# Optimization experiments

Measured on AMD Instinct MI355X. Metric: run time of the kernel, lower is better.

## Reference

```python
import jax, jax.numpy as jnp
import numpy as np

N = 8192
F_IN, F_HID, F_OUT = 256, 256, 64


def setup_inputs() -> dict:
    key = jax.random.key(0)
    k1, k2, k3, k4 = jax.random.split(key, 4)
    adj = jax.random.uniform(k1, (N, N), dtype=jnp.float32)
    x = jax.random.normal(k2, (N, F_IN), dtype=jnp.float32)
    W1 = jax.random.uniform(k3, (F_IN, F_HID), dtype=jnp.float32)
    W2 = jax.random.uniform(k4, (F_HID, F_OUT), dtype=jnp.float32)
    return {"adj": adj, "x": x, "W1": W1, "W2": W2}


def reference(adj, x, W1, W2):
    # Layer 1: left_to_right -> (adj @ x) @ W1, then ReLU (dropout is identity in eval)
    h = jnp.matmul(jnp.matmul(adj, x), W1)
    h = jax.nn.relu(h)
    # Layer 2 (last): no activation
    h = jnp.matmul(jnp.matmul(adj, h), W2)
    # Final log_softmax over class dim
    return jax.nn.log_softmax(h, axis=1)
```

## Files before the change

kernel.cpp:

```cpp
#include <hip/hip_runtime.h>

typedef short bf16x8 __attribute__((ext_vector_type(8)));
typedef float f32x4 __attribute__((ext_vector_type(4)));
typedef unsigned short us8 __attribute__((ext_vector_type(8)));

__device__ __forceinline__ unsigned short f2bf(float f) {
    unsigned int u = __float_as_uint(f);
    u += 0x7fffu + ((u >> 16) & 1u);
    return (unsigned short)(u >> 16);
}

__global__ __launch_bounds__(256) void transpose_cast_kernel(
    const float* __restrict__ in, unsigned short* __restrict__ out, int R, int Cc) {
    __shared__ alignas(16) unsigned short sT[64][65];
    const int r0 = blockIdx.x * 64, c0 = blockIdx.y * 64;
    const int t = threadIdx.x;
#pragma unroll
    for (int p = 0; p < 16; ++p) {
        int flat = p * 256 + t;
        int r = flat >> 6, c = flat & 63;
        sT[c][r] = f2bf(in[(size_t)(r0 + r) * Cc + (c0 + c)]);
    }
    __syncthreads();
#pragma unroll
    for (int p = 0; p < 16; ++p) {
        int flat = p * 256 + t;
        int c = flat >> 6, r = flat & 63;
        out[(size_t)(c0 + c) * R + (r0 + r)] = sT[c][r];
    }
}

template<int BN, int WM, int WN, int AMODE, bool TOUT, typename OutT>
__global__ __launch_bounds__(256) void gemm_kernel(
    const void* __restrict__ Aptr, const unsigned short* __restrict__ BT,
    OutT* __restrict__ C, int M, int N, int K, long aslab) {
    constexpr int BM = 64, BK = 64, LDW = 72;
    constexpr int MF = BM / WM / 16;
    constexpr int NF = BN / WN / 16;
    __shared__ alignas(16) unsigned short sA[BM * LDW];
    __shared__ alignas(16) unsigned short sB[BN * LDW];
    const int t = threadIdx.x;
    const int w = t >> 6, l = t & 63;
    const int wr = w / WN, wc = w % WN;
    const int m0 = blockIdx.x * BM;
    const int klen = K / gridDim.z;
    const int kbeg = blockIdx.z * klen;
    OutT* Cp = C + (size_t)blockIdx.z * M * N;

    f32x4 acc[MF][NF] = {};

    for (int k0 = kbeg; k0 < kbeg + klen; k0 += BK) {
        const float* A32 = (const float*)Aptr;
#pragma unroll
        for (int p = 0; p < 4; ++p) {
            int flat = p * 256 + t;
            int row = flat >> 4, c4 = flat & 15;
            size_t base = (size_t)(m0 + row) * K + k0 + c4 * 4;
            float4 v = *(const float4*)&A32[base];
            if constexpr (AMODE == 2) {
                float4 b = *(const float4*)&A32[aslab + base];
                float4 c = *(const float4*)&A32[2 * aslab + base];
                float4 d = *(const float4*)&A32[3 * aslab + base];
                v.x = fmaxf(v.x + b.x + c.x + d.x, 0.f);
                v.y = fmaxf(v.y + b.y + c.y + d.y, 0.f);
                v.z = fmaxf(v.z + b.z + c.z + d.z, 0.f);
                v.w = fmaxf(v.w + b.w + c.w + d.w, 0.f);
            }
            ushort4 o = make_ushort4(f2bf(v.x), f2bf(v.y), f2bf(v.z), f2bf(v.w));
            *(ushort4*)&sA[row * LDW + c4 * 4] = o;
        }
#pragma unroll
        for (int p = 0; p < BN * 8 / 256; ++p) {
            int flat = p * 256 + t;
            int row = flat >> 3, c8 = flat & 7;
            us8 v = *(const us8*)&BT[(size_t)row * K + k0 + c8 * 8];
            *(us8*)&sB[row * LDW + c8 * 8] = v;
        }
        __syncthreads();
#pragma unroll
        for (int kk = 0; kk < BK; kk += 32) {
            bf16x8 av[MF], bv[NF];
#pragma unroll
            for (int m = 0; m < MF; ++m)
                av[m] = *(const bf16x8*)&sA[(wr * (BM / WM) + m * 16 + (l & 15)) * LDW + kk + (l >> 4) * 8];
#pragma unroll
            for (int n = 0; n < NF; ++n)
                bv[n] = *(const bf16x8*)&sB[(wc * (BN / WN) + n * 16 + (l & 15)) * LDW + kk + (l >> 4) * 8];
#pragma unroll
            for (int m = 0; m < MF; ++m)
#pragma unroll
                for (int n = 0; n < NF; ++n)
                    acc[m][n] = __builtin_amdgcn_mfma_f32_16x16x32_bf16(av[m], bv[n], acc[m][n], 0, 0, 0);
        }
        __syncthreads();
    }

#pragma unroll
    for (int m = 0; m < MF; ++m) {
#pragma unroll
        for (int n = 0; n < NF; ++n) {
            const int col = wc * (BN / WN) + n * 16 + (l & 15);
            const int rb = m0 + wr * (BM / WM) + m * 16 + ((l >> 4) << 2);
            float v0 = acc[m][n][0], v1 = acc[m][n][1], v2 = acc[m][n][2], v3 = acc[m][n][3];
            if constexpr (TOUT) {
                ushort4 o = make_ushort4(f2bf(v0), f2bf(v1), f2bf(v2), f2bf(v3));
                *(ushort4*)((unsigned short*)Cp + (size_t)col * M + rb) = o;
            } else {
                Cp[(size_t)(rb + 0) * N + col] = (OutT)v0;
                Cp[(size_t)(rb + 1) * N + col] = (OutT)v1;
                Cp[(size_t)(rb + 2) * N + col] = (OutT)v2;
                Cp[(size_t)(rb + 3) * N + col] = (OutT)v3;
            }
        }
    }
}

template<int BN, int THREADS, int WM, int WN>
__global__ __launch_bounds__(THREADS, 4) void big_gemm_kernel(
    const float* __restrict__ A, const unsigned short* __restrict__ BT,
    float* __restrict__ C, int M, int N, int K) {
    constexpr int BM = 128, BK = 64, LDW = 72;
    constexpr int MF = BM / WM / 16, NF = BN / WN / 16;
    constexpr int ACH = (BM * BK / 4) / THREADS;
    constexpr int BCH = (BN * BK / 8) / THREADS;
    __shared__ alignas(16) unsigned short sA[2][BM * LDW];
    __shared__ alignas(16) unsigned short sB[2][BN * LDW];
    const int t = threadIdx.x, w = t >> 6, l = t & 63;
    const int wr = w / WN, wc = w % WN;
    const int m0 = blockIdx.x * BM;
    const int klen = K / gridDim.z, kbeg = blockIdx.z * klen;
    const int NT = klen / BK;
    float* Cp = C + (size_t)blockIdx.z * M * N;

    float4 ar[ACH];
    us8 br[BCH];

    auto LOAD = [&](int kc) {
#pragma unroll
        for (int p = 0; p < ACH; ++p) {
            int flat = p * THREADS + t, row = flat >> 4, c4 = flat & 15;
            ar[p] = *(const float4*)&A[(size_t)(m0 + row) * K + kc + c4 * 4];
        }
#pragma unroll
        for (int p = 0; p < BCH; ++p) {
            int flat = p * THREADS + t, row = flat >> 3, c8 = flat & 7;
            br[p] = *(const us8*)&BT[(size_t)row * K + kc + c8 * 8];
        }
    };
    auto WRITE = [&](int buf) {
#pragma unroll
        for (int p = 0; p < ACH; ++p) {
            int flat = p * THREADS + t, row = flat >> 4, c4 = flat & 15;
            float4 v = ar[p];
            *(ushort4*)&sA[buf][row * LDW + c4 * 4] =
                make_ushort4(f2bf(v.x), f2bf(v.y), f2bf(v.z), f2bf(v.w));
        }
#pragma unroll
        for (int p = 0; p < BCH; ++p) {
            int flat = p * THREADS + t, row = flat >> 3, c8 = flat & 7;
            *(us8*)&sB[buf][row * LDW + c8 * 8] = br[p];
        }
    };

    f32x4 acc[MF][NF] = {};
    LOAD(kbeg);
    WRITE(0);
    __syncthreads();
    int cur = 0;
    for (int tt = 0; tt < NT; ++tt) {
        if (tt + 1 < NT) LOAD(kbeg + (tt + 1) * BK);
#pragma unroll
        for (int kk = 0; kk < BK; kk += 32) {
            bf16x8 av[MF], bv[NF];
#pragma unroll
            for (int m = 0; m < MF; ++m)
                av[m] = *(const bf16x8*)&sA[cur][(wr * (BM / WM) + m * 16 + (l & 15)) * LDW + kk + (l >> 4) * 8];
#pragma unroll
            for (int n = 0; n < NF; ++n)
                bv[n] = *(const bf16x8*)&sB[cur][(wc * (BN / WN) + n * 16 + (l & 15)) * LDW + kk + (l >> 4) * 8];
#pragma unroll
            for (int m = 0; m < MF; ++m)
#pragma unroll
                for (int n = 0; n < NF; ++n)
                    acc[m][n] = __builtin_amdgcn_mfma_f32_16x16x32_bf16(av[m], bv[n], acc[m][n], 0, 0, 0);
        }
        if (tt + 1 < NT) {
            WRITE(cur ^ 1);
            __syncthreads();
            cur ^= 1;
        }
    }
#pragma unroll
    for (int m = 0; m < MF; ++m)
#pragma unroll
        for (int n = 0; n < NF; ++n) {
            const int col = wc * (BN / WN) + n * 16 + (l & 15);
            const int rb = m0 + wr * (BM / WM) + m * 16 + ((l >> 4) << 2);
#pragma unroll
            for (int j = 0; j < 4; ++j)
                Cp[(size_t)(rb + j) * N + col] = acc[m][n][j];
        }
}

__global__ __launch_bounds__(256) void head2_kernel(
    const float* __restrict__ p, float* __restrict__ out, int M) {
    const int t = threadIdx.x, w = t >> 6, l = t & 63;
    const size_t stride = (size_t)M * 64;
#pragma unroll
    for (int rr = 0; rr < 4; ++rr) {
        int i = blockIdx.x * 16 + w * 4 + rr;
        size_t off = (size_t)i * 64 + l;
        float v = 0.f;
#pragma unroll
        for (int s = 0; s < 8; ++s) v += p[s * stride + off];
        float mx = v;
#pragma unroll
        for (int o = 32; o; o >>= 1) mx = fmaxf(mx, __shfl_xor(mx, o));
        float d0 = v - mx;
        float e = __expf(d0);
#pragma unroll
        for (int o = 32; o; o >>= 1) e += __shfl_xor(e, o);
        out[off] = d0 - __logf(e);
    }
}

extern "C" void kernel_launch(void* const* d_in, const int* in_sizes, int n_in,
                              void* d_out, int out_size, void* d_ws, size_t ws_size,
                              hipStream_t stream) {
    const float* adj = (const float*)d_in[0];
    const float* x   = (const float*)d_in[1];
    const float* W1  = (const float*)d_in[2];
    const float* W2  = (const float*)d_in[3];
    float* out = (float*)d_out;

    const int M = 8192, K = 8192;
    char* ws = (char*)d_ws;
    float*          pbuf1 = (float*)ws;
    float*          pbuf2 = (float*)(ws + 33554432);
    unsigned short* zT    = (unsigned short*)(ws + 50331648);
    unsigned short* hwT   = (unsigned short*)(ws + 54525952);
    unsigned short* W1T   = (unsigned short*)(ws + 55574528);
    unsigned short* W2T   = (unsigned short*)(ws + 55705600);

    transpose_cast_kernel<<<dim3(4, 4), 256, 0, stream>>>(W1, W1T, 256, 256);
    transpose_cast_kernel<<<dim3(4, 1), 256, 0, stream>>>(W2, W2T, 256, 64);
    gemm_kernel<256, 1, 4, 1, true, unsigned short>
        <<<dim3(M / 64, 1, 1), 256, 0, stream>>>(x, W1T, zT, M, 256, 256, 0);
    big_gemm_kernel<256, 1024, 4, 4>
        <<<dim3(M / 128, 1, 4), 1024, 0, stream>>>(adj, zT, pbuf1, M, 256, K);
    gemm_kernel<64, 2, 2, 2, true, unsigned short>
        <<<dim3(M / 64, 1, 1), 256, 0, stream>>>(pbuf1, W2T, hwT, M, 64, 256, (long)M * 256);
    big_gemm_kernel<64, 512, 4, 2>
        <<<dim3(M / 128, 1, 8), 512, 0, stream>>>(adj, hwT, pbuf2, M, 64, K);
    head2_kernel<<<dim3(M / 16), 256, 0, stream>>>(pbuf2, out, M);
}
```

Baseline: 167.9 us.

## Stream fp32 adjacency tiles directly to LDS and convert to bf16 at fragment load

The big GEMM kernel now uses global_load_lds to copy fp32 adjacency tiles and bf16 B tiles straight into shared memory, with XOR-swizzled layouts, instead of staging them through registers. The fp32-to-bf16 conversion moves to the fragment-read stage using packed cvt instructions. Tile shapes change to BM=64, with a 512-thread block for both adjacency GEMMs. Double buffering is dropped for a single buffer with two barriers per k-step, which saves registers but exposes load latency unless occupancy hides it; fp32 staging also doubles the LDS traffic for A.

```diff
diff --git a/kernel.cpp b/kernel.cpp
--- a/kernel.cpp
+++ b/kernel.cpp
@@ -8,6 +8,20 @@
     unsigned int u = __float_as_uint(f);
     u += 0x7fffu + ((u >> 16) & 1u);
     return (unsigned short)(u >> 16);
+}
+
+__device__ __forceinline__ void gload16(const void* g, void* l) {
+    __builtin_amdgcn_global_load_lds((const __attribute__((address_space(1))) void*)g,
+                                     (__attribute__((address_space(3))) void*)l, 16, 0, 0);
+}
+
+__device__ __forceinline__ bf16x8 cvt_pk8(float4 a, float4 b) {
+    union { bf16x8 h; unsigned int u[4]; } r;
+    asm("v_cvt_pk_bf16_f32 %0, %1, %2" : "=v"(r.u[0]) : "v"(a.x), "v"(a.y));
+    asm("v_cvt_pk_bf16_f32 %0, %1, %2" : "=v"(r.u[1]) : "v"(a.z), "v"(a.w));
+    asm("v_cvt_pk_bf16_f32 %0, %1, %2" : "=v"(r.u[2]) : "v"(b.x), "v"(b.y));
+    asm("v_cvt_pk_bf16_f32 %0, %1, %2" : "=v"(r.u[3]) : "v"(b.z), "v"(b.w));
+    return r.h;
 }
 
 __global__ __launch_bounds__(256) void transpose_cast_kernel(
@@ -115,16 +129,17 @@
     }
 }
 
-template<int BN, int THREADS, int WM, int WN>
+template<int BM, int BN, int WM, int WN, int THREADS>
 __global__ __launch_bounds__(THREADS, 4) void big_gemm_kernel(
     const float* __restrict__ A, const unsigned short* __restrict__ BT,
     float* __restrict__ C, int M, int N, int K) {
-    constexpr int BM = 128, BK = 64, LDW = 72;
+    constexpr int BK = 64;
+    constexpr int NW = THREADS / 64;
     constexpr int MF = BM / WM / 16, NF = BN / WN / 16;
-    constexpr int ACH = (BM * BK / 4) / THREADS;
-    constexpr int BCH = (BN * BK / 8) / THREADS;
-    __shared__ alignas(16) unsigned short sA[2][BM * LDW];
-    __shared__ alignas(16) unsigned short sB[2][BN * LDW];
+    constexpr int AREG = BM * BK * 4 / 1024;
+    constexpr int BREG = BN * BK * 2 / 1024;
+    __shared__ alignas(16) float sA[BM * BK];
+    __shared__ alignas(16) unsigned short sB[BN * BK];
     const int t = threadIdx.x, w = t >> 6, l = t & 63;
     const int wr = w / WN, wc = w % WN;
     const int m0 = blockIdx.x * BM;
@@ -132,64 +147,51 @@
     const int NT = klen / BK;
     float* Cp = C + (size_t)blockIdx.z * M * N;
 
-    float4 ar[ACH];
-    us8 br[BCH];
-
-    auto LOAD = [&](int kc) {
-#pragma unroll
-        for (int p = 0; p < ACH; ++p) {
-            int flat = p * THREADS + t, row = flat >> 4, c4 = flat & 15;
-            ar[p] = *(const float4*)&A[(size_t)(m0 + row) * K + kc + c4 * 4];
-        }
-#pragma unroll
-        for (int p = 0; p < BCH; ++p) {
-            int flat = p * THREADS + t, row = flat >> 3, c8 = flat & 7;
-            br[p] = *(const us8*)&BT[(size_t)row * K + kc + c8 * 8];
-        }
-    };
-    auto WRITE = [&](int buf) {
-#pragma unroll
-        for (int p = 0; p < ACH; ++p) {
-            int flat = p * THREADS + t, row = flat >> 4, c4 = flat & 15;
-            float4 v = ar[p];
-            *(ushort4*)&sA[buf][row * LDW + c4 * 4] =
-                make_ushort4(f2bf(v.x), f2bf(v.y), f2bf(v.z), f2bf(v.w));
-        }
-#pragma unroll
-        for (int p = 0; p < BCH; ++p) {
-            int flat = p * THREADS + t, row = flat >> 3, c8 = flat & 7;
-            *(us8*)&sB[buf][row * LDW + c8 * 8] = br[p];
-        }
-    };
-
     f32x4 acc[MF][NF] = {};
-    LOAD(kbeg);
-    WRITE(0);
-    __syncthreads();
-    int cur = 0;
+
     for (int tt = 0; tt < NT; ++tt) {
-        if (tt + 1 < NT) LOAD(kbeg + (tt + 1) * BK);
+        const int k0 = kbeg + tt * BK;
+#pragma unroll
+        for (int j = 0; j < AREG / NW; ++j) {
+            int q = w + j * NW;
+            int r = q * 4 + (l >> 4);
+            int col = ((l & 15) ^ (r & 15)) * 4;
+            gload16(&A[(size_t)(m0 + r) * K + k0 + col], (char*)sA + q * 1024);
+        }
+#pragma unroll
+        for (int j = 0; j < BREG / NW; ++j) {
+            int q = w + j * NW;
+            int r = q * 8 + (l >> 3);
+            int col = ((l & 7) ^ (r & 7)) * 8;
+            gload16(&BT[(size_t)r * K + k0 + col], (char*)sB + q * 1024);
+        }
+        __syncthreads();
 #pragma unroll
         for (int kk = 0; kk < BK; kk += 32) {
             bf16x8 av[MF], bv[NF];
 #pragma unroll
-            for (int m = 0; m < MF; ++m)
-                av[m] = *(const bf16x8*)&sA[cur][(wr * (BM / WM) + m * 16 + (l & 15)) * LDW + kk + (l >> 4) * 8];
-#pragma unroll
-            for (int n = 0; n < NF; ++n)
-                bv[n] = *(const bf16x8*)&sB[cur][(wc * (BN / WN) + n * 16 + (l & 15)) * LDW + kk + (l >> 4) * 8];
+            for (int m = 0; m < MF; ++m) {
+                int r = wr * (BM / WM) + m * 16 + (l & 15);
+                int p0 = ((kk >> 2) + (l >> 4) * 2) ^ (r & 15);
+                float4 fa = *(const float4*)&sA[r * 64 + p0 * 4];
+                float4 fb = *(const float4*)&sA[r * 64 + (p0 ^ 1) * 4];
+                av[m] = cvt_pk8(fa, fb);
+            }
+#pragma unroll
+            for (int n = 0; n < NF; ++n) {
+                int r = wc * (BN / WN) + n * 16 + (l & 15);
+                int s = ((kk >> 3) + (l >> 4)) ^ (r & 7);
+                bv[n] = *(const bf16x8*)&sB[r * 64 + s * 8];
+            }
 #pragma unroll
             for (int m = 0; m < MF; ++m)
 #pragma unroll
                 for (int n = 0; n < NF; ++n)
                     acc[m][n] = __builtin_amdgcn_mfma_f32_16x16x32_bf16(av[m], bv[n], acc[m][n], 0, 0, 0);
         }
-        if (tt + 1 < NT) {
-            WRITE(cur ^ 1);
-            __syncthreads();
-            cur ^= 1;
-        }
-    }
+        __syncthreads();
+    }
+
 #pragma unroll
     for (int m = 0; m < MF; ++m)
 #pragma unroll
@@ -246,11 +248,11 @@
     transpose_cast_kernel<<<dim3(4, 1), 256, 0, stream>>>(W2, W2T, 256, 64);
     gemm_kernel<256, 1, 4, 1, true, unsigned short>
         <<<dim3(M / 64, 1, 1), 256, 0, stream>>>(x, W1T, zT, M, 256, 256, 0);
-    big_gemm_kernel<256, 1024, 4, 4>
-        <<<dim3(M / 128, 1, 4), 1024, 0, stream>>>(adj, zT, pbuf1, M, 256, K);
+    big_gemm_kernel<64, 256, 2, 4, 512>
+        <<<dim3(M / 64, 1, 4), 512, 0, stream>>>(adj, zT, pbuf1, M, 256, K);
     gemm_kernel<64, 2, 2, 2, true, unsigned short>
         <<<dim3(M / 64, 1, 1), 256, 0, stream>>>(pbuf1, W2T, hwT, M, 64, 256, (long)M * 256);
-    big_gemm_kernel<64, 512, 4, 2>
-        <<<dim3(M / 128, 1, 8), 512, 0, stream>>>(adj, hwT, pbuf2, M, 64, K);
+    big_gemm_kernel<64, 64, 4, 2, 512>
+        <<<dim3(M / 64, 1, 8), 512, 0, stream>>>(adj, hwT, pbuf2, M, 64, K);
     head2_kernel<<<dim3(M / 16), 256, 0, stream>>>(pbuf2, out, M);
 }
```

Result: slower. 175.7 us (+4.6%).
